# Performance work log

Hardware: AMD Instinct MI355X
Metric: run time of the kernel (lower is better)

Reference implementation:

```python
import jax, jax.numpy as jnp
import numpy as np

N_NODES = 50000
N_EDGES = 800000
IN_CH = 128
OUT_CH = 64
HEADS = 4
NEG_SLOPE = 0.2


def setup_inputs() -> dict:
    key = jax.random.key(0)
    k1, k2, k3, k4, k5, k6 = jax.random.split(key, 6)
    x = jax.random.normal(k1, (N_NODES, IN_CH), dtype=jnp.float32)
    edge_index = jax.random.randint(k2, (2, N_EDGES), 0, N_NODES, dtype=jnp.int64)
    # GATConv params (glorot-ish scale)
    W = jax.random.normal(k3, (HEADS * OUT_CH, IN_CH), dtype=jnp.float32) * (1.0 / np.sqrt(IN_CH))
    att_src = jax.random.normal(k4, (HEADS, OUT_CH), dtype=jnp.float32) * 0.1
    att_dst = jax.random.normal(k5, (HEADS, OUT_CH), dtype=jnp.float32) * 0.1
    bias = jax.random.normal(k6, (HEADS * OUT_CH,), dtype=jnp.float32) * 0.01
    return {"x": x, "edge_index": edge_index, "W": W, "att_src": att_src, "att_dst": att_dst, "bias": bias}


def reference(x, edge_index, W, att_src, att_dst, bias):
    N = x.shape[0]
    H, C = att_src.shape
    # add self loops (PyG GATConv default add_self_loops=True)
    loops = jnp.arange(N, dtype=edge_index.dtype)
    src = jnp.concatenate([edge_index[0], loops])  # [E+N]
    dst = jnp.concatenate([edge_index[1], loops])
    # linear projection -> [N, H, C]
    xl = (x @ W.T).reshape(N, H, C)
    # per-node attention logits [N, H]
    a_src = jnp.einsum('nhc,hc->nh', xl, att_src)
    a_dst = jnp.einsum('nhc,hc->nh', xl, att_dst)
    # edge-wise score, leaky relu
    alpha = jax.nn.leaky_relu(a_src[src] + a_dst[dst], NEG_SLOPE)  # [E+N, H]
    # segment softmax over destination nodes (every node has a self loop -> no empty segments)
    amax = jax.ops.segment_max(alpha, dst, num_segments=N)
    e = jnp.exp(alpha - amax[dst])
    denom = jax.ops.segment_sum(e, dst, num_segments=N)
    coef = e / denom[dst]  # [E+N, H]
    # weighted scatter-aggregate of source features
    out = jax.ops.segment_sum(coef[:, :, None] * xl[src], dst, num_segments=N)  # [N, H, C]
    out = out.reshape(N, H * C) + bias
    # last_layer=False -> ELU activation
    return jax.nn.elu(out)
```

## Files before the change

kernel.cpp:

```cpp
#include <hip/hip_runtime.h>
#include <hip/hip_bf16.h>
#include <math.h>

#define IN_C 128
#define HC   256
#define CH   64
#define NEG  0.2f

typedef __attribute__((ext_vector_type(8))) short short8;
typedef __attribute__((ext_vector_type(4))) float f32x4;

__device__ __forceinline__ float lrelu(float v) { return v > 0.f ? v : NEG * v; }

__device__ __forceinline__ unsigned short f2bf(float f) {
    __hip_bfloat16 h = __float2bfloat16(f);
    return *reinterpret_cast<unsigned short*>(&h);
}
__device__ __forceinline__ unsigned pack2(float lo, float hi) {
    return (unsigned)f2bf(lo) | ((unsigned)f2bf(hi) << 16);
}

__device__ __forceinline__ void fma8(float* acc, float w, const uint4 u) {
    acc[0] = fmaf(w, __uint_as_float(u.x << 16),        acc[0]);
    acc[1] = fmaf(w, __uint_as_float(u.x & 0xFFFF0000u), acc[1]);
    acc[2] = fmaf(w, __uint_as_float(u.y << 16),        acc[2]);
    acc[3] = fmaf(w, __uint_as_float(u.y & 0xFFFF0000u), acc[3]);
    acc[4] = fmaf(w, __uint_as_float(u.z << 16),        acc[4]);
    acc[5] = fmaf(w, __uint_as_float(u.z & 0xFFFF0000u), acc[5]);
    acc[6] = fmaf(w, __uint_as_float(u.w << 16),        acc[6]);
    acc[7] = fmaf(w, __uint_as_float(u.w & 0xFFFF0000u), acc[7]);
}

__global__ void k_wconv(const float* __restrict__ W, short* __restrict__ Wb, int n)
{
    int i = blockIdx.x * 256 + threadIdx.x;
    if (i * 4 >= n) return;
    const float4 v = *(const float4*)&W[i * 4];
    uint2 pk;
    pk.x = pack2(v.x, v.y);
    pk.y = pack2(v.z, v.w);
    *(uint2*)&Wb[i * 4] = pk;
}

__global__ void __launch_bounds__(256) k_gemm(
    const float* __restrict__ x, const short* __restrict__ Wb,
    const float* __restrict__ att_src, const float* __restrict__ att_dst,
    __hip_bfloat16* __restrict__ xlb, float* __restrict__ asrc,
    float* __restrict__ adst, int N)
{
    __shared__ short Wlds[256 * 128];

    const int t    = threadIdx.x;
    const int wv   = t >> 6;
    const int lane = t & 63;
    const int m    = lane & 15;
    const int quad = lane >> 4;
    const int r0   = blockIdx.x * 64 + wv * 16;

#pragma unroll
    for (int i = 0; i < 16; ++i) {
        const int g   = t + 256 * i;
        const int row = g >> 4;
        const int c   = g & 15;
        const uint4 v = *(const uint4*)&Wb[g * 8];
        *(uint4*)&Wlds[row * 128 + ((c ^ (row & 15)) * 8)] = v;
    }
    __syncthreads();

    f32x4 acc[16];
#pragma unroll
    for (int tc = 0; tc < 16; ++tc) acc[tc] = (f32x4){0.f, 0.f, 0.f, 0.f};

    const int arow = min(r0 + m, N - 1);
    const float* xrow = &x[(size_t)arow * IN_C];

#pragma unroll
    for (int kc = 0; kc < IN_C; kc += 32) {
        union { short8 v; unsigned u[4]; } a;
        const float4 xa = *(const float4*)&xrow[kc + quad * 8];
        const float4 xb = *(const float4*)&xrow[kc + quad * 8 + 4];
        a.u[0] = pack2(xa.x, xa.y); a.u[1] = pack2(xa.z, xa.w);
        a.u[2] = pack2(xb.x, xb.y); a.u[3] = pack2(xb.z, xb.w);
        const int kchunk = (kc >> 3) + quad;
        const int slotoff = ((kchunk ^ m) * 8);
#pragma unroll
        for (int tc = 0; tc < 16; ++tc) {
            const short8 b = *(const short8*)&Wlds[(tc * 16 + m) * 128 + slotoff];
            acc[tc] = __builtin_amdgcn_mfma_f32_16x16x32_bf16(a.v, b, acc[tc], 0, 0, 0);
        }
    }

    float as_l[16], ad_l[16];
#pragma unroll
    for (int tc = 0; tc < 16; ++tc) {
        as_l[tc] = att_src[tc * 16 + m];
        ad_l[tc] = att_dst[tc * 16 + m];
    }

#pragma unroll
    for (int i = 0; i < 4; ++i) {
        const int grow = r0 + quad * 4 + i;
        const bool ok = grow < N;
        float ps[4] = {0.f, 0.f, 0.f, 0.f};
        float pd[4] = {0.f, 0.f, 0.f, 0.f};
#pragma unroll
        for (int tc = 0; tc < 16; ++tc) {
            const float v = acc[tc][i];
            if (ok) xlb[(size_t)grow * HC + tc * 16 + m] = __float2bfloat16(v);
            ps[tc >> 2] = fmaf(v, as_l[tc], ps[tc >> 2]);
            pd[tc >> 2] = fmaf(v, ad_l[tc], pd[tc >> 2]);
        }
#pragma unroll
        for (int msk = 1; msk < 16; msk <<= 1) {
#pragma unroll
            for (int hd = 0; hd < 4; ++hd) {
                ps[hd] += __shfl_xor(ps[hd], msk);
                pd[hd] += __shfl_xor(pd[hd], msk);
            }
        }
        if (m == 0 && ok) {
#pragma unroll
            for (int hd = 0; hd < 4; ++hd) {
                asrc[grow * 4 + hd] = ps[hd];
                adst[grow * 4 + hd] = pd[hd];
            }
        }
    }
}

__global__ void k_deg(const int* __restrict__ ei, int* __restrict__ deg,
                      int* __restrict__ perm, int E)
{
    int e = blockIdx.x * 256 + threadIdx.x;
    if (e >= E) return;
    int d = ei[E + e];
    perm[e] = atomicAdd(&deg[d], 1);
}

__global__ void k_scan1(const int* __restrict__ deg, int* __restrict__ offs,
                        int* __restrict__ partials, int N)
{
    __shared__ int sh[1024];
    int t = threadIdx.x, b = blockIdx.x;
    int idx = b * 1024 + t;
    int v = (idx < N) ? deg[idx] : 0;
    sh[t] = v; __syncthreads();
    for (int off = 1; off < 1024; off <<= 1) {
        int u = (t >= off) ? sh[t - off] : 0;
        __syncthreads();
        sh[t] += u;
        __syncthreads();
    }
    if (idx < N) offs[idx] = sh[t] - v;
    if (t == 1023) partials[b] = sh[t];
}

__global__ void k_scan2(int* __restrict__ partials, int nparts)
{
    __shared__ int sh[1024];
    int t = threadIdx.x;
    int v = (t < nparts) ? partials[t] : 0;
    sh[t] = v; __syncthreads();
    for (int off = 1; off < 1024; off <<= 1) {
        int u = (t >= off) ? sh[t - off] : 0;
        __syncthreads();
        sh[t] += u;
        __syncthreads();
    }
    if (t < nparts) partials[t] = sh[t] - v;
}

__global__ void k_scan3(int* __restrict__ offs, const int* __restrict__ partials,
                        int N, int E)
{
    int t = threadIdx.x, b = blockIdx.x;
    int idx = b * 1024 + t;
    if (idx < N) offs[idx] += partials[b];
    if (idx == 0) offs[N] = E;
}

__global__ void k_place(const int* __restrict__ ei, const int* __restrict__ perm,
                        const int* __restrict__ offs, int* __restrict__ csr_src, int E)
{
    int e = blockIdx.x * 256 + threadIdx.x;
    if (e >= E) return;
    int s = ei[e];
    int d = ei[E + e];
    csr_src[offs[d] + perm[e]] = s;
}

__global__ void __launch_bounds__(256) k_agg(
    const __hip_bfloat16* __restrict__ xlb, const float* __restrict__ asrc,
    const float* __restrict__ adst, const int* __restrict__ offs,
    const int* __restrict__ csr_src, const float* __restrict__ bias,
    float* __restrict__ out, int N)
{
    const int t    = threadIdx.x;
    const int wv   = t >> 6;
    const int lane = t & 63;
    const int half = lane >> 5;
    const int li   = lane & 31;
    const int h    = li >> 3;
    const int n    = blockIdx.x * 4 + wv;
    if (n >= N) return;

    const float adn = adst[n * 4 + h];
    const int   p0 = offs[n];
    const int   pe = offs[n + 1];

    float acc[8];
#pragma unroll
    for (int q = 0; q < 8; ++q) acc[q] = 0.f;
    float l = 0.f;

    if (half == 0) {
        const float w = __expf(lrelu(asrc[n * 4 + h] + adn));
        const uint4 u = *(const uint4*)&xlb[(unsigned)n * HC + li * 8];
        fma8(acc, w, u);
        l = w;
    }

    int p = p0 + half;
    for (; p + 8 <= pe + half; p += 8) {
        const int s0 = csr_src[p];
        const int s1 = csr_src[p + 2];
        const int s2 = csr_src[p + 4];
        const int s3 = csr_src[p + 6];
        const float a0 = asrc[s0 * 4 + h];
        const float a1 = asrc[s1 * 4 + h];
        const float a2 = asrc[s2 * 4 + h];
        const float a3 = asrc[s3 * 4 + h];
        const uint4 u0 = *(const uint4*)&xlb[(unsigned)s0 * HC + li * 8];
        const uint4 u1 = *(const uint4*)&xlb[(unsigned)s1 * HC + li * 8];
        const uint4 u2 = *(const uint4*)&xlb[(unsigned)s2 * HC + li * 8];
        const uint4 u3 = *(const uint4*)&xlb[(unsigned)s3 * HC + li * 8];
        const float w0 = __expf(lrelu(a0 + adn));
        const float w1 = __expf(lrelu(a1 + adn));
        const float w2 = __expf(lrelu(a2 + adn));
        const float w3 = __expf(lrelu(a3 + adn));
        l += (w0 + w1) + (w2 + w3);
        fma8(acc, w0, u0);
        fma8(acc, w1, u1);
        fma8(acc, w2, u2);
        fma8(acc, w3, u3);
    }
    for (; p < pe; p += 2) {
        const int s0 = csr_src[p];
        const float a0 = asrc[s0 * 4 + h];
        const uint4 u0 = *(const uint4*)&xlb[(unsigned)s0 * HC + li * 8];
        const float w0 = __expf(lrelu(a0 + adn));
        l += w0;
        fma8(acc, w0, u0);
    }

    l += __shfl_xor(l, 32);
#pragma unroll
    for (int q = 0; q < 8; ++q) acc[q] += __shfl_xor(acc[q], 32);
    const float inv = 1.0f / l;

    const int cbase = li * 8 + half * 4;
    const float4 bv = *(const float4*)&bias[cbase];
    float4 o;
    o.x = acc[half * 4 + 0] * inv + bv.x;
    o.y = acc[half * 4 + 1] * inv + bv.y;
    o.z = acc[half * 4 + 2] * inv + bv.z;
    o.w = acc[half * 4 + 3] * inv + bv.w;
    o.x = o.x > 0.f ? o.x : expm1f(o.x);
    o.y = o.y > 0.f ? o.y : expm1f(o.y);
    o.z = o.z > 0.f ? o.z : expm1f(o.z);
    o.w = o.w > 0.f ? o.w : expm1f(o.w);
    *(float4*)&out[(size_t)n * HC + cbase] = o;
}

extern "C" void kernel_launch(void* const* d_in, const int* in_sizes, int n_in,
                              void* d_out, int out_size, void* d_ws, size_t ws_size,
                              hipStream_t stream) {
    const float* x       = (const float*)d_in[0];
    const int*   ei      = (const int*)d_in[1];
    const float* W       = (const float*)d_in[2];
    const float* att_src = (const float*)d_in[3];
    const float* att_dst = (const float*)d_in[4];
    const float* bias    = (const float*)d_in[5];
    float* out = (float*)d_out;

    const int N = in_sizes[0] / IN_C;
    const int E = in_sizes[1] / 2;
    const int W_ELEMS = HC * IN_C;

    char* p = (char*)d_ws;
    auto alloc = [&](size_t bytes) -> char* {
        char* q = p;
        p += (bytes + 255) & ~(size_t)255;
        return q;
    };
    __hip_bfloat16* xlb = (__hip_bfloat16*)alloc((size_t)N * HC * 2);
    short* Wb   = (short*)alloc((size_t)W_ELEMS * 2);
    float* asrc = (float*)alloc((size_t)N * 4 * 4);
    float* adst = (float*)alloc((size_t)N * 4 * 4);
    int*   deg  = (int*)alloc((size_t)N * 4);
    int*   offs = (int*)alloc((size_t)(N + 1) * 4);
    int*   perm = (int*)alloc((size_t)E * 4);
    int*   part = (int*)alloc(4096);
    int*   csr  = (int*)alloc((size_t)E * 4);

    hipMemsetAsync(deg, 0, (size_t)N * 4, stream);

    k_wconv<<<(W_ELEMS / 4 + 255) / 256, 256, 0, stream>>>(W, Wb, W_ELEMS);

    k_gemm<<<(N + 63) / 64, 256, 0, stream>>>(x, Wb, att_src, att_dst, xlb, asrc, adst, N);

    k_deg<<<(E + 255) / 256, 256, 0, stream>>>(ei, deg, perm, E);

    const int nb = (N + 1023) / 1024;
    k_scan1<<<nb, 1024, 0, stream>>>(deg, offs, part, N);
    k_scan2<<<1, 1024, 0, stream>>>(part, nb);
    k_scan3<<<nb, 1024, 0, stream>>>(offs, part, N, E);

    k_place<<<(E + 255) / 256, 256, 0, stream>>>(ei, perm, offs, csr, E);

    k_agg<<<(N + 3) / 4, 256, 0, stream>>>(xlb, asrc, adst, offs, csr, bias, out, N);
}
```

Before: 236.4 us.

## Store projected features head-major and split aggregation across heads in grid

The GEMM epilogue now writes the bf16 projected features and the per-node attention logits in a head-major layout ([H][N][C] and [H][N]). The aggregation kernel gets a second grid dimension over heads, so each wave handles one node-head pair. Within the wave, eight lanes share one edge's 64-channel slice and eight edges are processed at once, with the self loop folded into the edge loop. The aim is to make each gathered row per head a compact 128-byte read and to raise edge-level parallelism. In exchange, the csr/offs metadata is reread once per head and the final cross-lane reduction is longer.

```diff
diff --git a/kernel.cpp b/kernel.cpp
--- a/kernel.cpp
+++ b/kernel.cpp
@@ -106,7 +106,11 @@
 #pragma unroll
         for (int tc = 0; tc < 16; ++tc) {
             const float v = acc[tc][i];
-            if (ok) xlb[(size_t)grow * HC + tc * 16 + m] = __float2bfloat16(v);
+            if (ok) {
+                const int hd = tc >> 2;
+                const int ch = (tc & 3) * 16 + m;
+                xlb[((size_t)hd * N + grow) * CH + ch] = __float2bfloat16(v);
+            }
             ps[tc >> 2] = fmaf(v, as_l[tc], ps[tc >> 2]);
             pd[tc >> 2] = fmaf(v, ad_l[tc], pd[tc >> 2]);
         }
@@ -121,8 +125,8 @@
         if (m == 0 && ok) {
 #pragma unroll
             for (int hd = 0; hd < 4; ++hd) {
-                asrc[grow * 4 + hd] = ps[hd];
-                adst[grow * 4 + hd] = pd[hd];
+                asrc[(size_t)hd * N + grow] = ps[hd];
+                adst[(size_t)hd * N + grow] = pd[hd];
             }
         }
     }
@@ -198,78 +202,75 @@
     const int t    = threadIdx.x;
     const int wv   = t >> 6;
     const int lane = t & 63;
-    const int half = lane >> 5;
-    const int li   = lane & 31;
-    const int h    = li >> 3;
+    const int e8   = lane >> 3;
+    const int li   = lane & 7;
+    const int h    = blockIdx.y;
     const int n    = blockIdx.x * 4 + wv;
     if (n >= N) return;
 
-    const float adn = adst[n * 4 + h];
-    const int   p0 = offs[n];
-    const int   pe = offs[n + 1];
+    const __hip_bfloat16* __restrict__ xh = xlb + (size_t)h * N * CH;
+    const float* __restrict__ ah = asrc + (size_t)h * N;
+
+    const float adn = adst[(size_t)h * N + n];
+    const int p0  = offs[n];
+    const int cnt = offs[n + 1] - p0 + 1;
 
     float acc[8];
 #pragma unroll
     for (int q = 0; q < 8; ++q) acc[q] = 0.f;
     float l = 0.f;
 
-    if (half == 0) {
-        const float w = __expf(lrelu(asrc[n * 4 + h] + adn));
-        const uint4 u = *(const uint4*)&xlb[(unsigned)n * HC + li * 8];
-        fma8(acc, w, u);
-        l = w;
-    }
-
-    int p = p0 + half;
-    for (; p + 8 <= pe + half; p += 8) {
-        const int s0 = csr_src[p];
-        const int s1 = csr_src[p + 2];
-        const int s2 = csr_src[p + 4];
-        const int s3 = csr_src[p + 6];
-        const float a0 = asrc[s0 * 4 + h];
-        const float a1 = asrc[s1 * 4 + h];
-        const float a2 = asrc[s2 * 4 + h];
-        const float a3 = asrc[s3 * 4 + h];
-        const uint4 u0 = *(const uint4*)&xlb[(unsigned)s0 * HC + li * 8];
-        const uint4 u1 = *(const uint4*)&xlb[(unsigned)s1 * HC + li * 8];
-        const uint4 u2 = *(const uint4*)&xlb[(unsigned)s2 * HC + li * 8];
-        const uint4 u3 = *(const uint4*)&xlb[(unsigned)s3 * HC + li * 8];
+    int q = e8;
+    for (; q + 8 < cnt; q += 16) {
+        const int s0 = (q == 0) ? n : csr_src[p0 + q - 1];
+        const int s1 = csr_src[p0 + q + 7];
+        const float a0 = ah[s0];
+        const float a1 = ah[s1];
+        const uint4 u0 = *(const uint4*)&xh[(size_t)s0 * CH + li * 8];
+        const uint4 u1 = *(const uint4*)&xh[(size_t)s1 * CH + li * 8];
         const float w0 = __expf(lrelu(a0 + adn));
         const float w1 = __expf(lrelu(a1 + adn));
-        const float w2 = __expf(lrelu(a2 + adn));
-        const float w3 = __expf(lrelu(a3 + adn));
-        l += (w0 + w1) + (w2 + w3);
+        l += w0 + w1;
         fma8(acc, w0, u0);
         fma8(acc, w1, u1);
-        fma8(acc, w2, u2);
-        fma8(acc, w3, u3);
-    }
-    for (; p < pe; p += 2) {
-        const int s0 = csr_src[p];
-        const float a0 = asrc[s0 * 4 + h];
-        const uint4 u0 = *(const uint4*)&xlb[(unsigned)s0 * HC + li * 8];
+    }
+    if (q < cnt) {
+        const int s0 = (q == 0) ? n : csr_src[p0 + q - 1];
+        const float a0 = ah[s0];
+        const uint4 u0 = *(const uint4*)&xh[(size_t)s0 * CH + li * 8];
         const float w0 = __expf(lrelu(a0 + adn));
         l += w0;
         fma8(acc, w0, u0);
     }
 
-    l += __shfl_xor(l, 32);
-#pragma unroll
-    for (int q = 0; q < 8; ++q) acc[q] += __shfl_xor(acc[q], 32);
+#pragma unroll
+    for (int msk = 8; msk < 64; msk <<= 1) {
+        l += __shfl_xor(l, msk);
+#pragma unroll
+        for (int z = 0; z < 8; ++z) acc[z] += __shfl_xor(acc[z], msk);
+    }
     const float inv = 1.0f / l;
 
-    const int cbase = li * 8 + half * 4;
-    const float4 bv = *(const float4*)&bias[cbase];
-    float4 o;
-    o.x = acc[half * 4 + 0] * inv + bv.x;
-    o.y = acc[half * 4 + 1] * inv + bv.y;
-    o.z = acc[half * 4 + 2] * inv + bv.z;
-    o.w = acc[half * 4 + 3] * inv + bv.w;
-    o.x = o.x > 0.f ? o.x : expm1f(o.x);
-    o.y = o.y > 0.f ? o.y : expm1f(o.y);
-    o.z = o.z > 0.f ? o.z : expm1f(o.z);
-    o.w = o.w > 0.f ? o.w : expm1f(o.w);
-    *(float4*)&out[(size_t)n * HC + cbase] = o;
+    if (e8 == 0) {
+        const int cbase = h * CH + li * 8;
+        const float4 b0 = *(const float4*)&bias[cbase];
+        const float4 b1 = *(const float4*)&bias[cbase + 4];
+        float4 o0, o1;
+        o0.x = acc[0] * inv + b0.x; o0.y = acc[1] * inv + b0.y;
+        o0.z = acc[2] * inv + b0.z; o0.w = acc[3] * inv + b0.w;
+        o1.x = acc[4] * inv + b1.x; o1.y = acc[5] * inv + b1.y;
+        o1.z = acc[6] * inv + b1.z; o1.w = acc[7] * inv + b1.w;
+        o0.x = o0.x > 0.f ? o0.x : expm1f(o0.x);
+        o0.y = o0.y > 0.f ? o0.y : expm1f(o0.y);
+        o0.z = o0.z > 0.f ? o0.z : expm1f(o0.z);
+        o0.w = o0.w > 0.f ? o0.w : expm1f(o0.w);
+        o1.x = o1.x > 0.f ? o1.x : expm1f(o1.x);
+        o1.y = o1.y > 0.f ? o1.y : expm1f(o1.y);
+        o1.z = o1.z > 0.f ? o1.z : expm1f(o1.z);
+        o1.w = o1.w > 0.f ? o1.w : expm1f(o1.w);
+        *(float4*)&out[(size_t)n * HC + cbase]     = o0;
+        *(float4*)&out[(size_t)n * HC + cbase + 4] = o1;
+    }
 }
 
 extern "C" void kernel_launch(void* const* d_in, const int* in_sizes, int n_in,
@@ -318,5 +319,6 @@
 
     k_place<<<(E + 255) / 256, 256, 0, stream>>>(ei, perm, offs, csr, E);
 
-    k_agg<<<(N + 3) / 4, 256, 0, stream>>>(xlb, asrc, adst, offs, csr, bias, out, N);
-}
+    dim3 agrid((N + 3) / 4, 4, 1);
+    k_agg<<<agrid, 256, 0, stream>>>(xlb, asrc, adst, offs, csr, bias, out, N);
+}
```

Result: slower. 273.8 us (+15.9%).

## Fuse degree counting into GEMM launch and stage xl output through LDS

Applied to the files above, without the earlier changes.

Merges the degree-count kernel into the GEMM kernel by giving the first DB blocks a grid-stride loop over edges, so the atomic histogram overlaps with the projection GEMM and one launch is removed. The GEMM's bf16 output is now transposed through LDS (reusing the weight buffer with a padded stride) so each row goes out as coalesced 16-byte stores instead of scattered 2-byte stores. The aggregation kernel's output write becomes a nontemporal store. The change adds two block barriers and a block-type branch inside the GEMM kernel.

```diff
diff --git a/kernel.cpp b/kernel.cpp
--- a/kernel.cpp
+++ b/kernel.cpp
@@ -9,6 +9,8 @@
 
 typedef __attribute__((ext_vector_type(8))) short short8;
 typedef __attribute__((ext_vector_type(4))) float f32x4;
+
+#define TSTRIDE 264
 
 __device__ __forceinline__ float lrelu(float v) { return v > 0.f ? v : NEG * v; }
 
@@ -42,20 +44,32 @@
     *(uint2*)&Wb[i * 4] = pk;
 }
 
-__global__ void __launch_bounds__(256) k_gemm(
+__global__ void __launch_bounds__(256) k_gemm_deg(
     const float* __restrict__ x, const short* __restrict__ Wb,
     const float* __restrict__ att_src, const float* __restrict__ att_dst,
+    const int* __restrict__ ei, int* __restrict__ deg, int* __restrict__ perm,
     __hip_bfloat16* __restrict__ xlb, float* __restrict__ asrc,
-    float* __restrict__ adst, int N)
+    float* __restrict__ adst, int N, int E, int DB)
 {
     __shared__ short Wlds[256 * 128];
 
-    const int t    = threadIdx.x;
+    const int t = threadIdx.x;
+
+    if ((int)blockIdx.x < DB) {
+        const int stride = DB * 256;
+        for (int e = blockIdx.x * 256 + t; e < E; e += stride) {
+            const int d = ei[E + e];
+            perm[e] = atomicAdd(&deg[d], 1);
+        }
+        return;
+    }
+
+    const int bx   = blockIdx.x - DB;
     const int wv   = t >> 6;
     const int lane = t & 63;
     const int m    = lane & 15;
     const int quad = lane >> 4;
-    const int r0   = blockIdx.x * 64 + wv * 16;
+    const int r0   = bx * 64 + wv * 16;
 
 #pragma unroll
     for (int i = 0; i < 16; ++i) {
@@ -96,7 +110,6 @@
         as_l[tc] = att_src[tc * 16 + m];
         ad_l[tc] = att_dst[tc * 16 + m];
     }
-
 #pragma unroll
     for (int i = 0; i < 4; ++i) {
         const int grow = r0 + quad * 4 + i;
@@ -106,7 +119,6 @@
 #pragma unroll
         for (int tc = 0; tc < 16; ++tc) {
             const float v = acc[tc][i];
-            if (ok) xlb[(size_t)grow * HC + tc * 16 + m] = __float2bfloat16(v);
             ps[tc >> 2] = fmaf(v, as_l[tc], ps[tc >> 2]);
             pd[tc >> 2] = fmaf(v, ad_l[tc], pd[tc >> 2]);
         }
@@ -126,15 +138,27 @@
             }
         }
     }
-}
-
-__global__ void k_deg(const int* __restrict__ ei, int* __restrict__ deg,
-                      int* __restrict__ perm, int E)
-{
-    int e = blockIdx.x * 256 + threadIdx.x;
-    if (e >= E) return;
-    int d = ei[E + e];
-    perm[e] = atomicAdd(&deg[d], 1);
+
+    __syncthreads();
+#pragma unroll
+    for (int i = 0; i < 4; ++i) {
+        const int lrow = wv * 16 + quad * 4 + i;
+#pragma unroll
+        for (int tc = 0; tc < 16; ++tc)
+            Wlds[lrow * TSTRIDE + tc * 16 + m] = (short)f2bf(acc[tc][i]);
+    }
+    __syncthreads();
+    const int r0blk = bx * 64;
+#pragma unroll
+    for (int k2 = 0; k2 < 8; ++k2) {
+        const int c   = t + 256 * k2;
+        const int row = c >> 5;
+        const int off = c & 31;
+        if (r0blk + row < N) {
+            const uint4 v = *(const uint4*)&Wlds[row * TSTRIDE + off * 8];
+            *(uint4*)&xlb[(size_t)(r0blk + row) * HC + off * 8] = v;
+        }
+    }
 }
 
 __global__ void k_scan1(const int* __restrict__ deg, int* __restrict__ offs,
@@ -260,7 +284,7 @@
 
     const int cbase = li * 8 + half * 4;
     const float4 bv = *(const float4*)&bias[cbase];
-    float4 o;
+    f32x4 o;
     o.x = acc[half * 4 + 0] * inv + bv.x;
     o.y = acc[half * 4 + 1] * inv + bv.y;
     o.z = acc[half * 4 + 2] * inv + bv.z;
@@ -269,7 +293,7 @@
     o.y = o.y > 0.f ? o.y : expm1f(o.y);
     o.z = o.z > 0.f ? o.z : expm1f(o.z);
     o.w = o.w > 0.f ? o.w : expm1f(o.w);
-    *(float4*)&out[(size_t)n * HC + cbase] = o;
+    __builtin_nontemporal_store(o, (f32x4*)&out[(size_t)n * HC + cbase]);
 }
 
 extern "C" void kernel_launch(void* const* d_in, const int* in_sizes, int n_in,
@@ -303,13 +327,14 @@
     int*   part = (int*)alloc(4096);
     int*   csr  = (int*)alloc((size_t)E * 4);
 
-    hipMemsetAsync(deg, 0, (size_t)N * 4, stream);
+    (void)hipMemsetAsync(deg, 0, (size_t)N * 4, stream);
 
     k_wconv<<<(W_ELEMS / 4 + 255) / 256, 256, 0, stream>>>(W, Wb, W_ELEMS);
 
-    k_gemm<<<(N + 63) / 64, 256, 0, stream>>>(x, Wb, att_src, att_dst, xlb, asrc, adst, N);
-
-    k_deg<<<(E + 255) / 256, 256, 0, stream>>>(ei, deg, perm, E);
+    const int GB = (N + 63) / 64;
+    const int DB = (E + 2047) / 2048;
+    k_gemm_deg<<<DB + GB, 256, 0, stream>>>(x, Wb, att_src, att_dst,
+                                            ei, deg, perm, xlb, asrc, adst, N, E, DB);
 
     const int nb = (N + 1023) / 1024;
     k_scan1<<<nb, 1024, 0, stream>>>(deg, offs, part, N);
```

Result: faster. 224.6 us (-5.0%).
